# Kernel tuning notes

Measured on AMD Instinct MI355X. Metric: run time of the kernel, lower is better.

The kernel has to match this reference:

```python
import jax, jax.numpy as jnp
import numpy as np

N, D, E, TOP_K = 2048, 512, 16, 2
HID = 4 * D
EPS = 1e-10


def setup_inputs() -> dict:
    key = jax.random.key(0)
    ks = jax.random.split(key, 8)
    s = 0.02
    return {
        "x": jax.random.normal(ks[0], (N, D), dtype=jnp.float32),
        "w_norm": jnp.ones((D,), dtype=jnp.float32),
        "Wr": jax.random.normal(ks[1], (D, E), dtype=jnp.float32) * s,
        "br": jnp.zeros((E,), dtype=jnp.float32),
        "W1": jax.random.normal(ks[2], (E, D, HID), dtype=jnp.float32) * s,
        "b1": jnp.zeros((E, HID), dtype=jnp.float32),
        "W2": jax.random.normal(ks[3], (E, HID, D), dtype=jnp.float32) * s,
        "b2": jnp.zeros((E, D), dtype=jnp.float32),
    }


def reference(x, w_norm, Wr, br, W1, b1, W2, b2):
    res = x
    # RMSNorm over feature dim (dim=1 in the torch code for 2D input)
    rms = jnp.sqrt(jnp.mean(x * x, axis=1, keepdims=True) + EPS)
    xn = w_norm * (x / rms)
    # Router: top-k over expert logits, softmax over the k selected logits
    logits = xn @ Wr + br                      # [N, E]
    top_p, top_i = jax.lax.top_k(logits, TOP_K)  # [N, k]
    top_p = jax.nn.softmax(top_p, axis=-1)
    # Dense per-token expert weights [N, E] (top-k indices are distinct)
    weight = jnp.zeros((x.shape[0], E), dtype=x.dtype)
    weight = weight.at[jnp.arange(x.shape[0])[:, None], top_i].add(top_p)
    # All-expert FFN (dense reference for the routed dispatch)
    h = jnp.einsum("nd,edh->enh", xn, W1) + b1[:, None, :]   # [E, N, 4D]
    y = jnp.einsum("enh,ehd->end", jax.nn.silu(h), W2) + b2[:, None, :]  # [E, N, D]
    out = jnp.einsum("end,ne->nd", y, weight)
    return out + res
```

## Files before the change

### kernel.cpp

```cpp
#include <hip/hip_runtime.h>

#define N_TOK 2048
#define DIM   512
#define NEXP  16
#define HID   2048
#define NSLOT (N_TOK*2)

typedef __attribute__((ext_vector_type(8))) short short8;
typedef __attribute__((ext_vector_type(4))) float floatx4;

__device__ __forceinline__ ushort f2bf(float f) {
    union { float f; unsigned u; } c; c.f = f;
    unsigned u = c.u;
    unsigned r = (u + 0x7fffu + ((u >> 16) & 1u)) >> 16;
    return (ushort)r;
}
__device__ __forceinline__ float bf2f(ushort u) {
    union { unsigned u; float f; } c; c.u = ((unsigned)u) << 16;
    return c.f;
}

__device__ __forceinline__ void gl_lds16(const void* g, void* l) {
    __builtin_amdgcn_global_load_lds(
        (const __attribute__((address_space(1))) unsigned int*)g,
        (__attribute__((address_space(3))) unsigned int*)l, 16, 0, 0);
}

__global__ __launch_bounds__(256)
void transpose_convert(const float* __restrict__ src, ushort* __restrict__ dst,
                       int K, int Nn)
{
    const int NT = Nn >> 6, KT = K >> 6;
    int bx = blockIdx.x;
    const int nt = bx % NT; bx /= NT;
    const int kt = bx % KT; bx /= KT;
    const int e  = bx;

    __shared__ float Ls[64 * 65];
    const int t = threadIdx.x;

    const float* sp = src + ((size_t)e * K + kt * 64) * Nn + nt * 64;
#pragma unroll
    for (int i = 0; i < 4; i++) {
        const int k  = (t >> 4) + i * 16;
        const int c4 = (t & 15) * 4;
        const float4 v = *(const float4*)(sp + (size_t)k * Nn + c4);
        Ls[k * 65 + c4 + 0] = v.x;
        Ls[k * 65 + c4 + 1] = v.y;
        Ls[k * 65 + c4 + 2] = v.z;
        Ls[k * 65 + c4 + 3] = v.w;
    }
    __syncthreads();

    ushort* dp = dst + ((size_t)e * Nn + nt * 64) * K + kt * 64;
#pragma unroll
    for (int i = 0; i < 2; i++) {
        const int n = (t >> 3) + i * 32;
        const int c = t & 7;
        unsigned w[4];
#pragma unroll
        for (int q = 0; q < 4; q++) {
            const unsigned lo = f2bf(Ls[(c * 8 + q * 2 + 0) * 65 + n]);
            const unsigned hi = f2bf(Ls[(c * 8 + q * 2 + 1) * 65 + n]);
            w[q] = lo | (hi << 16);
        }
        uint4 o = make_uint4(w[0], w[1], w[2], w[3]);
        *(uint4*)(dp + (size_t)n * K + c * 8) = o;
    }
}

__global__ __launch_bounds__(256)
void router_fused(const float* __restrict__ x, const float* __restrict__ w_norm,
                  const float* __restrict__ Wr, const float* __restrict__ br,
                  ushort* __restrict__ xn, int2* __restrict__ rec_e,
                  float2* __restrict__ rec_w)
{
    __shared__ float xs[16][516];
    __shared__ float wrT[16][516];

    const int tid  = threadIdx.x;
    const int wave = tid >> 6, lane = tid & 63;
    const int tblk = blockIdx.x * 16;

#pragma unroll
    for (int k = 0; k < 32; k++) {
        const int idx = tid + k * 256;
        wrT[idx & 15][idx >> 4] = Wr[idx];
    }

    const float4* wnp = (const float4*)w_norm;
    const float4 wa = wnp[lane], wb = wnp[lane + 64];
#pragma unroll
    for (int i = 0; i < 4; i++) {
        const int tl = wave * 4 + i, t = tblk + tl;
        const float4* xp = (const float4*)(x + (size_t)t * DIM);
        const float4 a = xp[lane], b = xp[lane + 64];
        float ss = a.x*a.x + a.y*a.y + a.z*a.z + a.w*a.w
                 + b.x*b.x + b.y*b.y + b.z*b.z + b.w*b.w;
#pragma unroll
        for (int m = 32; m >= 1; m >>= 1) ss += __shfl_xor(ss, m, 64);
        const float rinv = 1.f / sqrtf(ss * (1.f / (float)DIM) + 1e-10f);
        float4 na, nb;
        na.x = a.x * wa.x * rinv; na.y = a.y * wa.y * rinv;
        na.z = a.z * wa.z * rinv; na.w = a.w * wa.w * rinv;
        nb.x = b.x * wb.x * rinv; nb.y = b.y * wb.y * rinv;
        nb.z = b.z * wb.z * rinv; nb.w = b.w * wb.w * rinv;
        *(float4*)&xs[tl][lane * 4]       = na;
        *(float4*)&xs[tl][256 + lane * 4] = nb;
        ushort4 ua, ub;
        ua.x = f2bf(na.x); ua.y = f2bf(na.y); ua.z = f2bf(na.z); ua.w = f2bf(na.w);
        ub.x = f2bf(nb.x); ub.y = f2bf(nb.y); ub.z = f2bf(nb.z); ub.w = f2bf(nb.w);
        ushort4* xo = (ushort4*)(xn + (size_t)t * DIM);
        xo[lane] = ua; xo[lane + 64] = ub;
    }
    __syncthreads();

    const int tl = tid >> 4, e = tid & 15;
    const int t = tblk + tl;
    float acc = 0.f;
#pragma unroll 4
    for (int d = 0; d < DIM; d += 4) {
        const float4 xv = *(const float4*)&xs[tl][d];
        const float4 wv = *(const float4*)&wrT[e][d];
        acc += xv.x * wv.x + xv.y * wv.y + xv.z * wv.z + xv.w * wv.w;
    }
    const float v = acc + br[e];

    float m0 = v; int i0 = e; float m1 = -1e30f; int i1 = 16;
#pragma unroll
    for (int msk = 1; msk < 16; msk <<= 1) {
        const float om0 = __shfl_xor(m0, msk, 64); const int oi0 = __shfl_xor(i0, msk, 64);
        const float om1 = __shfl_xor(m1, msk, 64); const int oi1 = __shfl_xor(i1, msk, 64);
        const bool bf_ = (om0 > m0) || (om0 == m0 && oi0 < i0);
        const float t0m = bf_ ? om0 : m0; const int t0i = bf_ ? oi0 : i0;
        const float l0m = bf_ ? m0 : om0; const int l0i = bf_ ? i0 : oi0;
        const bool b2_ = (om1 > m1) || (om1 == m1 && oi1 < i1);
        const float t2m = b2_ ? om1 : m1; const int t2i = b2_ ? oi1 : i1;
        const bool lw = (l0m > t2m) || (l0m == t2m && l0i < t2i);
        m0 = t0m; i0 = t0i;
        m1 = lw ? l0m : t2m; i1 = lw ? l0i : t2i;
    }
    if (e == 0) {
        const float ex = expf(m1 - m0);
        const float w0 = 1.f / (1.f + ex);
        rec_e[t] = make_int2(i0, i1);
        rec_w[t] = make_float2(w0, ex * w0);
    }
}

__global__ __launch_bounds__(1024)
void plan_kernel(const int2* __restrict__ rec_e, int* __restrict__ cnt,
                 int* __restrict__ off, int* __restrict__ tok_of_slot,
                 int* __restrict__ rec_slot)
{
    __shared__ int soff[17];
    const int e = threadIdx.x >> 6;
    const int lane = threadIdx.x & 63;

    int total = 0;
    for (int c = 0; c < N_TOK / 64; c++) {
        const int2 er = rec_e[c * 64 + lane];
        const bool hit = (er.x == e) || (er.y == e);
        total += __popcll(__ballot(hit));
    }
    if (lane == 0) soff[e + 1] = total;
    __syncthreads();
    if (threadIdx.x == 0) {
        soff[0] = 0;
        for (int q = 1; q <= 16; q++) soff[q] += soff[q - 1];
    }
    __syncthreads();
    int base = soff[e];
    if (lane == 0) { cnt[e] = soff[e + 1] - base; off[e] = base; }

    for (int c = 0; c < N_TOK / 64; c++) {
        const int t = c * 64 + lane;
        const int2 er = rec_e[t];
        const bool hit = (er.x == e) || (er.y == e);
        const unsigned long long b = __ballot(hit);
        if (hit) {
            const int slot = base + __popcll(b & ((1ull << lane) - 1ull));
            tok_of_slot[slot] = t;
            const int which = (er.y == e) ? 1 : 0;
            rec_slot[t * 2 + which] = slot;
        }
        base += __popcll(b);
    }
}

template<int MODE>
__global__ __launch_bounds__(256)
void gemm_expert(const ushort* __restrict__ A, int a_stride,
                 const ushort* __restrict__ WT, int wt_k,
                 const float* __restrict__ bias,
                 const int* __restrict__ cnt, const int* __restrict__ off,
                 const int* __restrict__ tok_of_slot,
                 ushort* __restrict__ hout, ushort* __restrict__ yout)
{
    const int flat = blockIdx.x + (blockIdx.y << 5);
    const int x = flat & 7;
    const int g = flat >> 3;
    int e, mt, nb, z;
    if (MODE == 0) {
        e  = x + ((g >> 7) << 3);
        const int r = g & 127;
        nb = r & 31; mt = r >> 5; z = 0;
    } else {
        const int G = ((g >> 5) << 3) + x;
        e = G >> 2; z = G & 3;
        const int idx = g & 31;
        mt = idx >> 3; nb = idx & 7;
    }

    const int count = cnt[e];
    if (mt * 128 >= count) return;
    const int base = off[e];
    const int rows = min(128, count - mt * 128);
    const int n0   = nb * 64;
    const int Nn   = (MODE == 0) ? HID : DIM;
    const int kbeg = (MODE == 0) ? 0 : (z * 512);
    ushort* yp = (MODE == 0) ? nullptr : (yout + (size_t)z * NSLOT * DIM);

    __shared__ __align__(16) ushort As[2][128 * 32];
    __shared__ __align__(16) ushort Bs[2][64 * 32];
    __shared__ int toks[128];

    const int tid = threadIdx.x;
    if (tid < 128) {
        const int r = tid < rows ? tid : rows - 1;
        const int slot = base + mt * 128 + r;
        toks[tid] = (MODE == 0) ? tok_of_slot[slot] : slot;
    }
    __syncthreads();

    const int lane = tid & 63;
    const int wid  = tid >> 6;
    const int wm = wid >> 1, wn = wid & 1;
    const int fr = lane & 15, fg = lane >> 4;

    const int rl  = lane >> 2;
    const int sko = ((lane & 3) ^ ((lane >> 4) & 3)) * 8;

    const ushort* aptr[2];
    const ushort* wbase = WT + (size_t)e * Nn * wt_k + (size_t)n0 * wt_k;
#pragma unroll
    for (int j = 0; j < 2; j++) {
        const int s = wid * 2 + j;
        aptr[j] = A + (size_t)toks[s * 16 + rl] * a_stride + sko;
    }
    const ushort* bptr = wbase + (size_t)(wid * 16 + rl) * wt_k + sko;

    floatx4 acc[4][2];
#pragma unroll
    for (int mi = 0; mi < 4; mi++)
#pragma unroll
        for (int ni = 0; ni < 2; ni++)
#pragma unroll
            for (int r = 0; r < 4; r++) acc[mi][ni][r] = 0.f;

#define STAGE(pb, k0)                                                        \
    do {                                                                     \
        _Pragma("unroll")                                                    \
        for (int j = 0; j < 2; j++)                                          \
            gl_lds16(aptr[j] + (k0), (void*)(&As[pb][(wid * 2 + j) * 512])); \
        gl_lds16(bptr + (k0), (void*)(&Bs[pb][wid * 512]));                  \
    } while (0)

    int cur = 0;
    STAGE(0, kbeg);

    const int cxor = (fr >> 2) & 3;
    for (int kt = 0; kt < 16; kt++) {
        if (kt < 15) {
            STAGE(cur ^ 1, kbeg + (kt + 1) * 32);
            asm volatile("s_waitcnt vmcnt(3)" ::: "memory");
        } else {
            asm volatile("s_waitcnt vmcnt(0)" ::: "memory");
        }
        __builtin_amdgcn_s_barrier();
        __builtin_amdgcn_sched_barrier(0);

        __builtin_amdgcn_s_setprio(1);
        {
            const int co = (fg ^ cxor) * 8;
            short8 af[4], bfr[2];
#pragma unroll
            for (int mi = 0; mi < 4; mi++)
                af[mi] = *(const short8*)&As[cur][(wm * 64 + mi * 16 + fr) * 32 + co];
#pragma unroll
            for (int ni = 0; ni < 2; ni++)
                bfr[ni] = *(const short8*)&Bs[cur][(wn * 32 + ni * 16 + fr) * 32 + co];
#pragma unroll
            for (int mi = 0; mi < 4; mi++)
#pragma unroll
                for (int ni = 0; ni < 2; ni++)
                    acc[mi][ni] = __builtin_amdgcn_mfma_f32_16x16x32_bf16(af[mi], bfr[ni], acc[mi][ni], 0, 0, 0);
        }
        __builtin_amdgcn_s_setprio(0);

        __builtin_amdgcn_sched_barrier(0);
        __builtin_amdgcn_s_barrier();
        cur ^= 1;
    }
#undef STAGE

#pragma unroll
    for (int ni = 0; ni < 2; ni++) {
        const int gn = n0 + wn * 32 + ni * 16 + fr;
        const float bv = (MODE == 0) ? bias[e * HID + gn] : 0.f;
#pragma unroll
        for (int mi = 0; mi < 4; mi++) {
#pragma unroll
            for (int r = 0; r < 4; r++) {
                const int lm = wm * 64 + mi * 16 + fg * 4 + r;
                if (lm < rows) {
                    const int slot = base + mt * 128 + lm;
                    float v = acc[mi][ni][r];
                    if (MODE == 0) {
                        v += bv;
                        v = v / (1.f + __expf(-v));
                        hout[(size_t)slot * HID + gn] = f2bf(v);
                    } else {
                        yp[(size_t)slot * DIM + gn] = f2bf(v);
                    }
                }
            }
        }
    }
}

__global__ __launch_bounds__(128)
void gather_kernel(const float* __restrict__ x, const ushort* __restrict__ ypart,
                   const float* __restrict__ b2,
                   const int2* __restrict__ rec_e, const float2* __restrict__ rec_w,
                   const int2* __restrict__ rec_slot, float* __restrict__ out)
{
    const int t = blockIdx.x;
    const int d4 = threadIdx.x * 4;
    const int2 ei = rec_e[t];
    const float2 w = rec_w[t];
    const int2 sl = rec_slot[t];
    const float4 xv  = *(const float4*)(x  + (size_t)t * DIM + d4);
    float4 s0 = make_float4(0.f, 0.f, 0.f, 0.f);
    float4 s1 = make_float4(0.f, 0.f, 0.f, 0.f);
#pragma unroll
    for (int kc = 0; kc < 4; kc++) {
        const ushort* yp = ypart + (size_t)kc * NSLOT * DIM;
        const ushort4 a = *(const ushort4*)(yp + (size_t)sl.x * DIM + d4);
        const ushort4 b = *(const ushort4*)(yp + (size_t)sl.y * DIM + d4);
        s0.x += bf2f(a.x); s0.y += bf2f(a.y); s0.z += bf2f(a.z); s0.w += bf2f(a.w);
        s1.x += bf2f(b.x); s1.y += bf2f(b.y); s1.z += bf2f(b.z); s1.w += bf2f(b.w);
    }
    const float4 b0  = *(const float4*)(b2 + (size_t)ei.x * DIM + d4);
    const float4 b1v = *(const float4*)(b2 + (size_t)ei.y * DIM + d4);
    float4 o;
    o.x = xv.x + w.x * (s0.x + b0.x) + w.y * (s1.x + b1v.x);
    o.y = xv.y + w.x * (s0.y + b0.y) + w.y * (s1.y + b1v.y);
    o.z = xv.z + w.x * (s0.z + b0.z) + w.y * (s1.z + b1v.z);
    o.w = xv.w + w.x * (s0.w + b0.w) + w.y * (s1.w + b1v.w);
    *(float4*)(out + (size_t)t * DIM + d4) = o;
}

extern "C" void kernel_launch(void* const* d_in, const int* in_sizes, int n_in,
                              void* d_out, int out_size, void* d_ws, size_t ws_size,
                              hipStream_t stream)
{
    const float* x  = (const float*)d_in[0];
    const float* wn = (const float*)d_in[1];
    const float* Wr = (const float*)d_in[2];
    const float* br = (const float*)d_in[3];
    const float* W1 = (const float*)d_in[4];
    const float* b1 = (const float*)d_in[5];
    const float* W2 = (const float*)d_in[6];
    const float* b2 = (const float*)d_in[7];
    float* out = (float*)d_out;

    char* ws = (char*)d_ws;
    ushort* W1T   = (ushort*)(ws);
    ushort* W2T   = (ushort*)(ws + (32u << 20));
    ushort* xn    = (ushort*)(ws + (64u << 20));
    ushort* h_buf = (ushort*)(ws + (66u << 20));
    ushort* y_par = (ushort*)(ws + (82u << 20));
    char* p = ws + (114u << 20);
    int*    cnt         = (int*)p;    p += 256;
    int*    off         = (int*)p;    p += 256;
    int2*   rec_e       = (int2*)p;   p += N_TOK * 8;
    float2* rec_w       = (float2*)p; p += N_TOK * 8;
    int2*   rec_slot    = (int2*)p;   p += N_TOK * 8;
    int*    tok_of_slot = (int*)p;    p += NSLOT * 4;

    router_fused<<<N_TOK / 16, 256, 0, stream>>>(x, wn, Wr, br, xn, rec_e, rec_w);
    plan_kernel<<<1, 1024, 0, stream>>>(rec_e, cnt, off, tok_of_slot, (int*)rec_slot);

    transpose_convert<<<NEXP * 8 * 32, 256, 0, stream>>>(W1, W1T, DIM, HID);
    gemm_expert<0><<<dim3(32, 64), 256, 0, stream>>>(
        xn, DIM, W1T, DIM, b1, cnt, off, tok_of_slot, h_buf, nullptr);

    transpose_convert<<<NEXP * 32 * 8, 256, 0, stream>>>(W2, W2T, HID, DIM);
    gemm_expert<1><<<dim3(32, 64), 256, 0, stream>>>(
        h_buf, HID, W2T, HID, nullptr, cnt, off, nullptr, nullptr, y_par);

    gather_kernel<<<N_TOK, 128, 0, stream>>>(x, y_par, b2, rec_e, rec_w, rec_slot, out);
}
```

Baseline: 117.0 us.

## Fuse weight transposes into plan and GEMM1 launches to overlap independent work

The W1 transpose-convert is merged into the single-block plan kernel as extra blocks, and the W2 transpose-convert is appended as extra blocks to the first expert GEMM launch. This cuts two kernel launches and lets the independent transpose work run alongside the serial planning block and the GEMM1 tiles. Shared memory is now a raw byte buffer shared between the two roles. The plan block now uses 256 threads handling 4 experts per wave, so it runs longer on one block, and GEMM1 blocks may compete with the transpose blocks for CUs.

```diff
diff --git a/kernel.cpp b/kernel.cpp
--- a/kernel.cpp
+++ b/kernel.cpp
@@ -26,17 +26,16 @@
         (__attribute__((address_space(3))) unsigned int*)l, 16, 0, 0);
 }
 
-__global__ __launch_bounds__(256)
-void transpose_convert(const float* __restrict__ src, ushort* __restrict__ dst,
-                       int K, int Nn)
-{
-    const int NT = Nn >> 6, KT = K >> 6;
-    int bx = blockIdx.x;
+__device__ __forceinline__ void transpose_tile(const float* __restrict__ src,
+                                               ushort* __restrict__ dst,
+                                               int K, int Nn, int bx, void* smem)
+{
+    float* Ls = (float*)smem;
+    const int NT = Nn >> 6;
+    const int KT = K >> 6;
     const int nt = bx % NT; bx /= NT;
     const int kt = bx % KT; bx /= KT;
     const int e  = bx;
-
-    __shared__ float Ls[64 * 65];
     const int t = threadIdx.x;
 
     const float* sp = src + ((size_t)e * K + kt * 64) * Nn + nt * 64;
@@ -148,56 +147,71 @@
     }
 }
 
-__global__ __launch_bounds__(1024)
-void plan_kernel(const int2* __restrict__ rec_e, int* __restrict__ cnt,
-                 int* __restrict__ off, int* __restrict__ tok_of_slot,
-                 int* __restrict__ rec_slot)
-{
-    __shared__ int soff[17];
-    const int e = threadIdx.x >> 6;
-    const int lane = threadIdx.x & 63;
-
-    int total = 0;
-    for (int c = 0; c < N_TOK / 64; c++) {
-        const int2 er = rec_e[c * 64 + lane];
-        const bool hit = (er.x == e) || (er.y == e);
-        total += __popcll(__ballot(hit));
-    }
-    if (lane == 0) soff[e + 1] = total;
+__global__ __launch_bounds__(256)
+void plan_trw1_kernel(const int2* __restrict__ rec_e, int* __restrict__ cnt,
+                      int* __restrict__ off, int* __restrict__ tok_of_slot,
+                      int* __restrict__ rec_slot,
+                      const float* __restrict__ w1src, ushort* __restrict__ w1dst)
+{
+    __shared__ __align__(16) char smem[16640];
+
+    if (blockIdx.x != 0) {
+        transpose_tile(w1src, w1dst, DIM, HID, blockIdx.x - 1, smem);
+        return;
+    }
+
+    int* soff = (int*)smem;
+    const int tid = threadIdx.x;
+    const int wv = tid >> 6, lane = tid & 63;
+
+#pragma unroll
+    for (int s = 0; s < 4; s++) {
+        const int e = wv * 4 + s;
+        int total = 0;
+        for (int c = 0; c < N_TOK / 64; c++) {
+            const int2 er = rec_e[c * 64 + lane];
+            const bool hit = (er.x == e) || (er.y == e);
+            total += __popcll(__ballot(hit));
+        }
+        if (lane == 0) soff[e + 1] = total;
+    }
     __syncthreads();
-    if (threadIdx.x == 0) {
+    if (tid == 0) {
         soff[0] = 0;
         for (int q = 1; q <= 16; q++) soff[q] += soff[q - 1];
     }
     __syncthreads();
-    int base = soff[e];
-    if (lane == 0) { cnt[e] = soff[e + 1] - base; off[e] = base; }
-
-    for (int c = 0; c < N_TOK / 64; c++) {
-        const int t = c * 64 + lane;
-        const int2 er = rec_e[t];
-        const bool hit = (er.x == e) || (er.y == e);
-        const unsigned long long b = __ballot(hit);
-        if (hit) {
-            const int slot = base + __popcll(b & ((1ull << lane) - 1ull));
-            tok_of_slot[slot] = t;
-            const int which = (er.y == e) ? 1 : 0;
-            rec_slot[t * 2 + which] = slot;
-        }
-        base += __popcll(b);
+
+#pragma unroll
+    for (int s = 0; s < 4; s++) {
+        const int e = wv * 4 + s;
+        int base = soff[e];
+        if (lane == 0) { cnt[e] = soff[e + 1] - base; off[e] = base; }
+        for (int c = 0; c < N_TOK / 64; c++) {
+            const int t = c * 64 + lane;
+            const int2 er = rec_e[t];
+            const bool hit = (er.x == e) || (er.y == e);
+            const unsigned long long b = __ballot(hit);
+            if (hit) {
+                const int slot = base + __popcll(b & ((1ull << lane) - 1ull));
+                tok_of_slot[slot] = t;
+                const int which = (er.y == e) ? 1 : 0;
+                rec_slot[t * 2 + which] = slot;
+            }
+            base += __popcll(b);
+        }
     }
 }
 
 template<int MODE>
-__global__ __launch_bounds__(256)
-void gemm_expert(const ushort* __restrict__ A, int a_stride,
+__device__ __forceinline__ void gemm_body(const ushort* __restrict__ A, int a_stride,
                  const ushort* __restrict__ WT, int wt_k,
                  const float* __restrict__ bias,
                  const int* __restrict__ cnt, const int* __restrict__ off,
                  const int* __restrict__ tok_of_slot,
-                 ushort* __restrict__ hout, ushort* __restrict__ yout)
-{
-    const int flat = blockIdx.x + (blockIdx.y << 5);
+                 ushort* __restrict__ hout, ushort* __restrict__ yout,
+                 int flat, void* smem)
+{
     const int x = flat & 7;
     const int g = flat >> 3;
     int e, mt, nb, z;
@@ -221,9 +235,9 @@
     const int kbeg = (MODE == 0) ? 0 : (z * 512);
     ushort* yp = (MODE == 0) ? nullptr : (yout + (size_t)z * NSLOT * DIM);
 
-    __shared__ __align__(16) ushort As[2][128 * 32];
-    __shared__ __align__(16) ushort Bs[2][64 * 32];
-    __shared__ int toks[128];
+    ushort* As_ = (ushort*)smem;
+    ushort* Bs_ = (ushort*)((char*)smem + 16384);
+    int*    toks = (int*)((char*)smem + 24576);
 
     const int tid = threadIdx.x;
     if (tid < 128) {
@@ -258,12 +272,12 @@
 #pragma unroll
             for (int r = 0; r < 4; r++) acc[mi][ni][r] = 0.f;
 
-#define STAGE(pb, k0)                                                        \
-    do {                                                                     \
-        _Pragma("unroll")                                                    \
-        for (int j = 0; j < 2; j++)                                          \
-            gl_lds16(aptr[j] + (k0), (void*)(&As[pb][(wid * 2 + j) * 512])); \
-        gl_lds16(bptr + (k0), (void*)(&Bs[pb][wid * 512]));                  \
+#define STAGE(pb, k0)                                                              \
+    do {                                                                           \
+        _Pragma("unroll")                                                          \
+        for (int j = 0; j < 2; j++)                                                \
+            gl_lds16(aptr[j] + (k0), (void*)(&As_[(pb) * 4096 + (wid * 2 + j) * 512])); \
+        gl_lds16(bptr + (k0), (void*)(&Bs_[(pb) * 2048 + wid * 512]));             \
     } while (0)
 
     int cur = 0;
@@ -286,10 +300,10 @@
             short8 af[4], bfr[2];
 #pragma unroll
             for (int mi = 0; mi < 4; mi++)
-                af[mi] = *(const short8*)&As[cur][(wm * 64 + mi * 16 + fr) * 32 + co];
+                af[mi] = *(const short8*)&As_[cur * 4096 + (wm * 64 + mi * 16 + fr) * 32 + co];
 #pragma unroll
             for (int ni = 0; ni < 2; ni++)
-                bfr[ni] = *(const short8*)&Bs[cur][(wn * 32 + ni * 16 + fr) * 32 + co];
+                bfr[ni] = *(const short8*)&Bs_[cur * 2048 + (wn * 32 + ni * 16 + fr) * 32 + co];
 #pragma unroll
             for (int mi = 0; mi < 4; mi++)
 #pragma unroll
@@ -329,6 +343,38 @@
     }
 }
 
+__global__ __launch_bounds__(256)
+void gemm1_trw2_kernel(const ushort* __restrict__ A,
+                       const ushort* __restrict__ W1T,
+                       const float* __restrict__ b1,
+                       const int* __restrict__ cnt, const int* __restrict__ off,
+                       const int* __restrict__ tok_of_slot,
+                       ushort* __restrict__ hout,
+                       const float* __restrict__ w2src, ushort* __restrict__ w2dst)
+{
+    __shared__ __align__(16) char smem[25088];
+    if (blockIdx.y >= 64) {
+        const int bx = (blockIdx.y - 64) * 32 + blockIdx.x;
+        transpose_tile(w2src, w2dst, HID, DIM, bx, smem);
+        return;
+    }
+    const int flat = blockIdx.x + (blockIdx.y << 5);
+    gemm_body<0>(A, DIM, W1T, DIM, b1, cnt, off, tok_of_slot, hout, nullptr,
+                 flat, smem);
+}
+
+__global__ __launch_bounds__(256)
+void gemm2_kernel(const ushort* __restrict__ A,
+                  const ushort* __restrict__ W2T,
+                  const int* __restrict__ cnt, const int* __restrict__ off,
+                  ushort* __restrict__ yout)
+{
+    __shared__ __align__(16) char smem[25088];
+    const int flat = blockIdx.x + (blockIdx.y << 5);
+    gemm_body<1>(A, HID, W2T, HID, nullptr, cnt, off, nullptr, nullptr, yout,
+                 flat, smem);
+}
+
 __global__ __launch_bounds__(128)
 void gather_kernel(const float* __restrict__ x, const ushort* __restrict__ ypart,
                    const float* __restrict__ b2,
@@ -390,15 +436,14 @@
     int*    tok_of_slot = (int*)p;    p += NSLOT * 4;
 
     router_fused<<<N_TOK / 16, 256, 0, stream>>>(x, wn, Wr, br, xn, rec_e, rec_w);
-    plan_kernel<<<1, 1024, 0, stream>>>(rec_e, cnt, off, tok_of_slot, (int*)rec_slot);
-
-    transpose_convert<<<NEXP * 8 * 32, 256, 0, stream>>>(W1, W1T, DIM, HID);
-    gemm_expert<0><<<dim3(32, 64), 256, 0, stream>>>(
-        xn, DIM, W1T, DIM, b1, cnt, off, tok_of_slot, h_buf, nullptr);
-
-    transpose_convert<<<NEXP * 32 * 8, 256, 0, stream>>>(W2, W2T, HID, DIM);
-    gemm_expert<1><<<dim3(32, 64), 256, 0, stream>>>(
-        h_buf, HID, W2T, HID, nullptr, cnt, off, nullptr, nullptr, y_par);
+
+    plan_trw1_kernel<<<1 + NEXP * 8 * 32, 256, 0, stream>>>(
+        rec_e, cnt, off, tok_of_slot, (int*)rec_slot, W1, W1T);
+
+    gemm1_trw2_kernel<<<dim3(32, 192), 256, 0, stream>>>(
+        xn, W1T, b1, cnt, off, tok_of_slot, h_buf, W2, W2T);
+
+    gemm2_kernel<<<dim3(32, 64), 256, 0, stream>>>(h_buf, W2T, cnt, off, y_par);
 
     gather_kernel<<<N_TOK, 128, 0, stream>>>(x, y_par, b2, rec_e, rec_w, rec_slot, out);
 }
```

After: 116.2 us. About the same (-0.7%).

## Fuse weight fp32-to-bf16 conversion into expert GEMMs, drop transpose kernels

Applied to the files above, without the earlier changes.

Removes the two transpose_convert passes that wrote bf16 transposed copies of W1 and W2 to workspace. The expert GEMMs now stream fp32 weights straight from the original [K,N] layout into shared memory and convert them to bf16 per element while building the MFMA B fragments. This saves a full extra read and write of both weight tensors and two launches. In exchange it doubles the bytes of weight traffic per tile and adds scalar LDS reads and conversions inside the MFMA loop.

```diff
diff --git a/kernel.cpp b/kernel.cpp
--- a/kernel.cpp
+++ b/kernel.cpp
@@ -24,49 +24,6 @@
     __builtin_amdgcn_global_load_lds(
         (const __attribute__((address_space(1))) unsigned int*)g,
         (__attribute__((address_space(3))) unsigned int*)l, 16, 0, 0);
-}
-
-__global__ __launch_bounds__(256)
-void transpose_convert(const float* __restrict__ src, ushort* __restrict__ dst,
-                       int K, int Nn)
-{
-    const int NT = Nn >> 6, KT = K >> 6;
-    int bx = blockIdx.x;
-    const int nt = bx % NT; bx /= NT;
-    const int kt = bx % KT; bx /= KT;
-    const int e  = bx;
-
-    __shared__ float Ls[64 * 65];
-    const int t = threadIdx.x;
-
-    const float* sp = src + ((size_t)e * K + kt * 64) * Nn + nt * 64;
-#pragma unroll
-    for (int i = 0; i < 4; i++) {
-        const int k  = (t >> 4) + i * 16;
-        const int c4 = (t & 15) * 4;
-        const float4 v = *(const float4*)(sp + (size_t)k * Nn + c4);
-        Ls[k * 65 + c4 + 0] = v.x;
-        Ls[k * 65 + c4 + 1] = v.y;
-        Ls[k * 65 + c4 + 2] = v.z;
-        Ls[k * 65 + c4 + 3] = v.w;
-    }
-    __syncthreads();
-
-    ushort* dp = dst + ((size_t)e * Nn + nt * 64) * K + kt * 64;
-#pragma unroll
-    for (int i = 0; i < 2; i++) {
-        const int n = (t >> 3) + i * 32;
-        const int c = t & 7;
-        unsigned w[4];
-#pragma unroll
-        for (int q = 0; q < 4; q++) {
-            const unsigned lo = f2bf(Ls[(c * 8 + q * 2 + 0) * 65 + n]);
-            const unsigned hi = f2bf(Ls[(c * 8 + q * 2 + 1) * 65 + n]);
-            w[q] = lo | (hi << 16);
-        }
-        uint4 o = make_uint4(w[0], w[1], w[2], w[3]);
-        *(uint4*)(dp + (size_t)n * K + c * 8) = o;
-    }
 }
 
 __global__ __launch_bounds__(256)
@@ -190,12 +147,12 @@
 
 template<int MODE>
 __global__ __launch_bounds__(256)
-void gemm_expert(const ushort* __restrict__ A, int a_stride,
-                 const ushort* __restrict__ WT, int wt_k,
-                 const float* __restrict__ bias,
-                 const int* __restrict__ cnt, const int* __restrict__ off,
-                 const int* __restrict__ tok_of_slot,
-                 ushort* __restrict__ hout, ushort* __restrict__ yout)
+void gemm_f32b(const ushort* __restrict__ A, int a_stride,
+               const float* __restrict__ W, int NnW, int Ktot,
+               const float* __restrict__ bias,
+               const int* __restrict__ cnt, const int* __restrict__ off,
+               const int* __restrict__ tok_of_slot,
+               ushort* __restrict__ hout, ushort* __restrict__ yout)
 {
     const int flat = blockIdx.x + (blockIdx.y << 5);
     const int x = flat & 7;
@@ -217,12 +174,11 @@
     const int base = off[e];
     const int rows = min(128, count - mt * 128);
     const int n0   = nb * 64;
-    const int Nn   = (MODE == 0) ? HID : DIM;
     const int kbeg = (MODE == 0) ? 0 : (z * 512);
     ushort* yp = (MODE == 0) ? nullptr : (yout + (size_t)z * NSLOT * DIM);
 
     __shared__ __align__(16) ushort As[2][128 * 32];
-    __shared__ __align__(16) ushort Bs[2][64 * 32];
+    __shared__ __align__(16) float  Bf[2][32 * 64];
     __shared__ int toks[128];
 
     const int tid = threadIdx.x;
@@ -242,13 +198,18 @@
     const int sko = ((lane & 3) ^ ((lane >> 4) & 3)) * 8;
 
     const ushort* aptr[2];
-    const ushort* wbase = WT + (size_t)e * Nn * wt_k + (size_t)n0 * wt_k;
 #pragma unroll
     for (int j = 0; j < 2; j++) {
         const int s = wid * 2 + j;
-        aptr[j] = A + (size_t)toks[s * 16 + rl] * a_stride + sko;
-    }
-    const ushort* bptr = wbase + (size_t)(wid * 16 + rl) * wt_k + sko;
+        aptr[j] = A + (size_t)toks[s * 16 + rl] * a_stride + kbeg + sko;
+    }
+    const float* bptr[2];
+#pragma unroll
+    for (int j = 0; j < 2; j++) {
+        const int s = wid * 2 + j;
+        bptr[j] = W + ((size_t)e * Ktot + kbeg + s * 4 + (lane >> 4)) * NnW
+                    + n0 + (lane & 15) * 4;
+    }
 
     floatx4 acc[4][2];
 #pragma unroll
@@ -258,22 +219,27 @@
 #pragma unroll
             for (int r = 0; r < 4; r++) acc[mi][ni][r] = 0.f;
 
-#define STAGE(pb, k0)                                                        \
-    do {                                                                     \
-        _Pragma("unroll")                                                    \
-        for (int j = 0; j < 2; j++)                                          \
-            gl_lds16(aptr[j] + (k0), (void*)(&As[pb][(wid * 2 + j) * 512])); \
-        gl_lds16(bptr + (k0), (void*)(&Bs[pb][wid * 512]));                  \
+#define STAGE(pb, ktn)                                                             \
+    do {                                                                           \
+        const int ka = (ktn) * 32;                                                 \
+        const size_t kb = (size_t)(ktn) * 32 * NnW;                                \
+        _Pragma("unroll")                                                          \
+        for (int j = 0; j < 2; j++)                                                \
+            gl_lds16(aptr[j] + ka, (void*)(&As[pb][(wid * 2 + j) * 512]));         \
+        _Pragma("unroll")                                                          \
+        for (int j = 0; j < 2; j++)                                                \
+            gl_lds16(bptr[j] + kb, (void*)(&Bf[pb][(wid * 2 + j) * 256]));         \
     } while (0)
 
     int cur = 0;
-    STAGE(0, kbeg);
+    STAGE(0, 0);
 
     const int cxor = (fr >> 2) & 3;
+    const int bcol = wn * 32 + fr;
     for (int kt = 0; kt < 16; kt++) {
         if (kt < 15) {
-            STAGE(cur ^ 1, kbeg + (kt + 1) * 32);
-            asm volatile("s_waitcnt vmcnt(3)" ::: "memory");
+            STAGE(cur ^ 1, kt + 1);
+            asm volatile("s_waitcnt vmcnt(4)" ::: "memory");
         } else {
             asm volatile("s_waitcnt vmcnt(0)" ::: "memory");
         }
@@ -288,8 +254,13 @@
             for (int mi = 0; mi < 4; mi++)
                 af[mi] = *(const short8*)&As[cur][(wm * 64 + mi * 16 + fr) * 32 + co];
 #pragma unroll
-            for (int ni = 0; ni < 2; ni++)
-                bfr[ni] = *(const short8*)&Bs[cur][(wn * 32 + ni * 16 + fr) * 32 + co];
+            for (int ni = 0; ni < 2; ni++) {
+#pragma unroll
+                for (int j = 0; j < 8; j++) {
+                    const float f = Bf[cur][(fg * 8 + j) * 64 + bcol + ni * 16];
+                    bfr[ni][j] = (short)f2bf(f);
+                }
+            }
 #pragma unroll
             for (int mi = 0; mi < 4; mi++)
 #pragma unroll
@@ -376,12 +347,10 @@
     float* out = (float*)d_out;
 
     char* ws = (char*)d_ws;
-    ushort* W1T   = (ushort*)(ws);
-    ushort* W2T   = (ushort*)(ws + (32u << 20));
-    ushort* xn    = (ushort*)(ws + (64u << 20));
-    ushort* h_buf = (ushort*)(ws + (66u << 20));
-    ushort* y_par = (ushort*)(ws + (82u << 20));
-    char* p = ws + (114u << 20);
+    ushort* xn    = (ushort*)(ws);
+    ushort* h_buf = (ushort*)(ws + (2u  << 20));
+    ushort* y_par = (ushort*)(ws + (18u << 20));
+    char* p = ws + (40u << 20);
     int*    cnt         = (int*)p;    p += 256;
     int*    off         = (int*)p;    p += 256;
     int2*   rec_e       = (int2*)p;   p += N_TOK * 8;
@@ -390,15 +359,14 @@
     int*    tok_of_slot = (int*)p;    p += NSLOT * 4;
 
     router_fused<<<N_TOK / 16, 256, 0, stream>>>(x, wn, Wr, br, xn, rec_e, rec_w);
+
     plan_kernel<<<1, 1024, 0, stream>>>(rec_e, cnt, off, tok_of_slot, (int*)rec_slot);
 
-    transpose_convert<<<NEXP * 8 * 32, 256, 0, stream>>>(W1, W1T, DIM, HID);
-    gemm_expert<0><<<dim3(32, 64), 256, 0, stream>>>(
-        xn, DIM, W1T, DIM, b1, cnt, off, tok_of_slot, h_buf, nullptr);
-
-    transpose_convert<<<NEXP * 32 * 8, 256, 0, stream>>>(W2, W2T, HID, DIM);
-    gemm_expert<1><<<dim3(32, 64), 256, 0, stream>>>(
-        h_buf, HID, W2T, HID, nullptr, cnt, off, nullptr, nullptr, y_par);
+    gemm_f32b<0><<<dim3(32, 64), 256, 0, stream>>>(
+        xn, DIM, W1, HID, DIM, b1, cnt, off, tok_of_slot, h_buf, nullptr);
+
+    gemm_f32b<1><<<dim3(32, 64), 256, 0, stream>>>(
+        h_buf, HID, W2, DIM, HID, nullptr, cnt, off, nullptr, nullptr, y_par);
 
     gather_kernel<<<N_TOK, 128, 0, stream>>>(x, y_par, b2, rec_e, rec_w, rec_slot, out);
 }
```

Result: faster. 107.1 us (-8.5%).

## Read fp32 W1 directly in GEMM1 and fuse W2 transpose into same launch

Applied to the files above, without the earlier changes.

Removes the separate W1 transpose/convert pass. GEMM1 now streams fp32 W1 tiles straight into LDS and converts them to bf16 per element while building MFMA fragments. The W2 transpose/convert is folded into the GEMM1 launch as extra blocks, so it can overlap with GEMM1 work and one launch is dropped. The cost is twice the LDS bytes for B, scalar LDS reads plus conversion in the inner loop, and a larger shared-memory footprint that may reduce occupancy.

```diff
diff --git a/kernel.cpp b/kernel.cpp
--- a/kernel.cpp
+++ b/kernel.cpp
@@ -26,17 +26,16 @@
         (__attribute__((address_space(3))) unsigned int*)l, 16, 0, 0);
 }
 
-__global__ __launch_bounds__(256)
-void transpose_convert(const float* __restrict__ src, ushort* __restrict__ dst,
-                       int K, int Nn)
-{
-    const int NT = Nn >> 6, KT = K >> 6;
-    int bx = blockIdx.x;
+__device__ __forceinline__ void transpose_tile(const float* __restrict__ src,
+                                               ushort* __restrict__ dst,
+                                               int K, int Nn, int bx, void* smem)
+{
+    float* Ls = (float*)smem;
+    const int NT = Nn >> 6;
+    const int KT = K >> 6;
     const int nt = bx % NT; bx /= NT;
     const int kt = bx % KT; bx /= KT;
     const int e  = bx;
-
-    __shared__ float Ls[64 * 65];
     const int t = threadIdx.x;
 
     const float* sp = src + ((size_t)e * K + kt * 64) * Nn + nt * 64;
@@ -188,48 +187,43 @@
     }
 }
 
-template<int MODE>
 __global__ __launch_bounds__(256)
-void gemm_expert(const ushort* __restrict__ A, int a_stride,
-                 const ushort* __restrict__ WT, int wt_k,
-                 const float* __restrict__ bias,
-                 const int* __restrict__ cnt, const int* __restrict__ off,
-                 const int* __restrict__ tok_of_slot,
-                 ushort* __restrict__ hout, ushort* __restrict__ yout)
-{
+void gemm1_trw2(const ushort* __restrict__ A,
+                const float* __restrict__ W1, const float* __restrict__ b1,
+                const int* __restrict__ cnt, const int* __restrict__ off,
+                const int* __restrict__ tok_of_slot,
+                ushort* __restrict__ hout,
+                const float* __restrict__ w2src, ushort* __restrict__ w2dst)
+{
+    __shared__ __align__(16) char smem[33280];
+
+    if (blockIdx.y >= 64) {
+        const int bx = (blockIdx.y - 64) * 32 + blockIdx.x;
+        transpose_tile(w2src, w2dst, HID, DIM, bx, smem);
+        return;
+    }
+
     const int flat = blockIdx.x + (blockIdx.y << 5);
     const int x = flat & 7;
     const int g = flat >> 3;
-    int e, mt, nb, z;
-    if (MODE == 0) {
-        e  = x + ((g >> 7) << 3);
-        const int r = g & 127;
-        nb = r & 31; mt = r >> 5; z = 0;
-    } else {
-        const int G = ((g >> 5) << 3) + x;
-        e = G >> 2; z = G & 3;
-        const int idx = g & 31;
-        mt = idx >> 3; nb = idx & 7;
-    }
+    const int e  = x + ((g >> 7) << 3);
+    const int r0_ = g & 127;
+    const int nb = r0_ & 31, mt = r0_ >> 5;
 
     const int count = cnt[e];
     if (mt * 128 >= count) return;
     const int base = off[e];
     const int rows = min(128, count - mt * 128);
     const int n0   = nb * 64;
-    const int Nn   = (MODE == 0) ? HID : DIM;
-    const int kbeg = (MODE == 0) ? 0 : (z * 512);
-    ushort* yp = (MODE == 0) ? nullptr : (yout + (size_t)z * NSLOT * DIM);
-
-    __shared__ __align__(16) ushort As[2][128 * 32];
-    __shared__ __align__(16) ushort Bs[2][64 * 32];
-    __shared__ int toks[128];
+
+    ushort* As_ = (ushort*)smem;
+    float*  Bf_ = (float*)(smem + 16384);
+    int*    toks = (int*)(smem + 32768);
 
     const int tid = threadIdx.x;
     if (tid < 128) {
         const int r = tid < rows ? tid : rows - 1;
-        const int slot = base + mt * 128 + r;
-        toks[tid] = (MODE == 0) ? tok_of_slot[slot] : slot;
+        toks[tid] = tok_of_slot[base + mt * 128 + r];
     }
     __syncthreads();
 
@@ -242,13 +236,18 @@
     const int sko = ((lane & 3) ^ ((lane >> 4) & 3)) * 8;
 
     const ushort* aptr[2];
-    const ushort* wbase = WT + (size_t)e * Nn * wt_k + (size_t)n0 * wt_k;
 #pragma unroll
     for (int j = 0; j < 2; j++) {
         const int s = wid * 2 + j;
-        aptr[j] = A + (size_t)toks[s * 16 + rl] * a_stride + sko;
-    }
-    const ushort* bptr = wbase + (size_t)(wid * 16 + rl) * wt_k + sko;
+        aptr[j] = A + (size_t)toks[s * 16 + rl] * DIM + sko;
+    }
+    const float* bptr[2];
+#pragma unroll
+    for (int j = 0; j < 2; j++) {
+        const int s = wid * 2 + j;
+        const int cs = ((lane & 15) * 4) ^ (((s >> 1) & 1) << 4);
+        bptr[j] = W1 + ((size_t)e * DIM + s * 4 + (lane >> 4)) * HID + n0 + cs;
+    }
 
     floatx4 acc[4][2];
 #pragma unroll
@@ -258,7 +257,142 @@
 #pragma unroll
             for (int r = 0; r < 4; r++) acc[mi][ni][r] = 0.f;
 
-#define STAGE(pb, k0)                                                        \
+#define STAGE1(pb, ktn)                                                            \
+    do {                                                                           \
+        const int ka = (ktn) * 32;                                                 \
+        const size_t kb = (size_t)(ktn) * 32 * HID;                                \
+        _Pragma("unroll")                                                          \
+        for (int j = 0; j < 2; j++)                                                \
+            gl_lds16(aptr[j] + ka, (void*)(&As_[(pb) * 4096 + (wid * 2 + j) * 512])); \
+        _Pragma("unroll")                                                          \
+        for (int j = 0; j < 2; j++)                                                \
+            gl_lds16(bptr[j] + kb, (void*)(&Bf_[(pb) * 2048 + (wid * 2 + j) * 256])); \
+    } while (0)
+
+    int cur = 0;
+    STAGE1(0, 0);
+
+    const int cxor = (fr >> 2) & 3;
+    const int bbase = wn * 32 + fr;
+    const int fgx = fg & 1;
+    for (int kt = 0; kt < 16; kt++) {
+        if (kt < 15) {
+            STAGE1(cur ^ 1, kt + 1);
+            asm volatile("s_waitcnt vmcnt(4)" ::: "memory");
+        } else {
+            asm volatile("s_waitcnt vmcnt(0)" ::: "memory");
+        }
+        __builtin_amdgcn_s_barrier();
+        __builtin_amdgcn_sched_barrier(0);
+
+        __builtin_amdgcn_s_setprio(1);
+        {
+            const int co = (fg ^ cxor) * 8;
+            short8 af[4], bfr[2];
+#pragma unroll
+            for (int mi = 0; mi < 4; mi++)
+                af[mi] = *(const short8*)&As_[cur * 4096 + (wm * 64 + mi * 16 + fr) * 32 + co];
+#pragma unroll
+            for (int ni = 0; ni < 2; ni++) {
+                const int pcol = bbase + ((ni ^ fgx) << 4);
+#pragma unroll
+                for (int j = 0; j < 8; j++) {
+                    const float f = Bf_[cur * 2048 + (fg * 8 + j) * 64 + pcol];
+                    bfr[ni][j] = (short)f2bf(f);
+                }
+            }
+#pragma unroll
+            for (int mi = 0; mi < 4; mi++)
+#pragma unroll
+                for (int ni = 0; ni < 2; ni++)
+                    acc[mi][ni] = __builtin_amdgcn_mfma_f32_16x16x32_bf16(af[mi], bfr[ni], acc[mi][ni], 0, 0, 0);
+        }
+        __builtin_amdgcn_s_setprio(0);
+
+        __builtin_amdgcn_sched_barrier(0);
+        __builtin_amdgcn_s_barrier();
+        cur ^= 1;
+    }
+#undef STAGE1
+
+#pragma unroll
+    for (int ni = 0; ni < 2; ni++) {
+        const int gn = n0 + wn * 32 + ni * 16 + fr;
+        const float bv = b1[e * HID + gn];
+#pragma unroll
+        for (int mi = 0; mi < 4; mi++) {
+#pragma unroll
+            for (int r = 0; r < 4; r++) {
+                const int lm = wm * 64 + mi * 16 + fg * 4 + r;
+                if (lm < rows) {
+                    const int slot = base + mt * 128 + lm;
+                    float v = acc[mi][ni][r] + bv;
+                    v = v / (1.f + __expf(-v));
+                    hout[(size_t)slot * HID + gn] = f2bf(v);
+                }
+            }
+        }
+    }
+}
+
+__global__ __launch_bounds__(256)
+void gemm2_kernel(const ushort* __restrict__ A,
+                  const ushort* __restrict__ WT,
+                  const int* __restrict__ cnt, const int* __restrict__ off,
+                  ushort* __restrict__ yout)
+{
+    const int flat = blockIdx.x + (blockIdx.y << 5);
+    const int x = flat & 7;
+    const int g = flat >> 3;
+    const int G = ((g >> 5) << 3) + x;
+    const int e = G >> 2, z = G & 3;
+    const int idx = g & 31;
+    const int mt = idx >> 3, nb = idx & 7;
+
+    const int count = cnt[e];
+    if (mt * 128 >= count) return;
+    const int base = off[e];
+    const int rows = min(128, count - mt * 128);
+    const int n0   = nb * 64;
+    const int kbeg = z * 512;
+    ushort* yp = yout + (size_t)z * NSLOT * DIM;
+
+    __shared__ __align__(16) ushort As[2][128 * 32];
+    __shared__ __align__(16) ushort Bs[2][64 * 32];
+    __shared__ int toks[128];
+
+    const int tid = threadIdx.x;
+    if (tid < 128) {
+        const int r = tid < rows ? tid : rows - 1;
+        toks[tid] = base + mt * 128 + r;
+    }
+    __syncthreads();
+
+    const int lane = tid & 63;
+    const int wid  = tid >> 6;
+    const int wm = wid >> 1, wn = wid & 1;
+    const int fr = lane & 15, fg = lane >> 4;
+
+    const int rl  = lane >> 2;
+    const int sko = ((lane & 3) ^ ((lane >> 4) & 3)) * 8;
+
+    const ushort* aptr[2];
+#pragma unroll
+    for (int j = 0; j < 2; j++) {
+        const int s = wid * 2 + j;
+        aptr[j] = A + (size_t)toks[s * 16 + rl] * HID + kbeg + sko;
+    }
+    const ushort* bptr = WT + ((size_t)e * DIM + n0 + wid * 16 + rl) * HID + kbeg + sko;
+
+    floatx4 acc[4][2];
+#pragma unroll
+    for (int mi = 0; mi < 4; mi++)
+#pragma unroll
+        for (int ni = 0; ni < 2; ni++)
+#pragma unroll
+            for (int r = 0; r < 4; r++) acc[mi][ni][r] = 0.f;
+
+#define STAGE2(pb, k0)                                                       \
     do {                                                                     \
         _Pragma("unroll")                                                    \
         for (int j = 0; j < 2; j++)                                          \
@@ -267,12 +401,12 @@
     } while (0)
 
     int cur = 0;
-    STAGE(0, kbeg);
+    STAGE2(0, 0);
 
     const int cxor = (fr >> 2) & 3;
     for (int kt = 0; kt < 16; kt++) {
         if (kt < 15) {
-            STAGE(cur ^ 1, kbeg + (kt + 1) * 32);
+            STAGE2(cur ^ 1, (kt + 1) * 32);
             asm volatile("s_waitcnt vmcnt(3)" ::: "memory");
         } else {
             asm volatile("s_waitcnt vmcnt(0)" ::: "memory");
@@ -302,12 +436,11 @@
         __builtin_amdgcn_s_barrier();
         cur ^= 1;
     }
-#undef STAGE
+#undef STAGE2
 
 #pragma unroll
     for (int ni = 0; ni < 2; ni++) {
         const int gn = n0 + wn * 32 + ni * 16 + fr;
-        const float bv = (MODE == 0) ? bias[e * HID + gn] : 0.f;
 #pragma unroll
         for (int mi = 0; mi < 4; mi++) {
 #pragma unroll
@@ -315,14 +448,7 @@
                 const int lm = wm * 64 + mi * 16 + fg * 4 + r;
                 if (lm < rows) {
                     const int slot = base + mt * 128 + lm;
-                    float v = acc[mi][ni][r];
-                    if (MODE == 0) {
-                        v += bv;
-                        v = v / (1.f + __expf(-v));
-                        hout[(size_t)slot * HID + gn] = f2bf(v);
-                    } else {
-                        yp[(size_t)slot * DIM + gn] = f2bf(v);
-                    }
+                    yp[(size_t)slot * DIM + gn] = f2bf(acc[mi][ni][r]);
                 }
             }
         }
@@ -376,12 +502,11 @@
     float* out = (float*)d_out;
 
     char* ws = (char*)d_ws;
-    ushort* W1T   = (ushort*)(ws);
-    ushort* W2T   = (ushort*)(ws + (32u << 20));
-    ushort* xn    = (ushort*)(ws + (64u << 20));
-    ushort* h_buf = (ushort*)(ws + (66u << 20));
-    ushort* y_par = (ushort*)(ws + (82u << 20));
-    char* p = ws + (114u << 20);
+    ushort* W2T   = (ushort*)(ws);
+    ushort* xn    = (ushort*)(ws + (32u << 20));
+    ushort* h_buf = (ushort*)(ws + (34u << 20));
+    ushort* y_par = (ushort*)(ws + (50u << 20));
+    char* p = ws + (80u << 20);
     int*    cnt         = (int*)p;    p += 256;
     int*    off         = (int*)p;    p += 256;
     int2*   rec_e       = (int2*)p;   p += N_TOK * 8;
@@ -390,15 +515,13 @@
     int*    tok_of_slot = (int*)p;    p += NSLOT * 4;
 
     router_fused<<<N_TOK / 16, 256, 0, stream>>>(x, wn, Wr, br, xn, rec_e, rec_w);
+
     plan_kernel<<<1, 1024, 0, stream>>>(rec_e, cnt, off, tok_of_slot, (int*)rec_slot);
 
-    transpose_convert<<<NEXP * 8 * 32, 256, 0, stream>>>(W1, W1T, DIM, HID);
-    gemm_expert<0><<<dim3(32, 64), 256, 0, stream>>>(
-        xn, DIM, W1T, DIM, b1, cnt, off, tok_of_slot, h_buf, nullptr);
-
-    transpose_convert<<<NEXP * 32 * 8, 256, 0, stream>>>(W2, W2T, HID, DIM);
-    gemm_expert<1><<<dim3(32, 64), 256, 0, stream>>>(
-        h_buf, HID, W2T, HID, nullptr, cnt, off, nullptr, nullptr, y_par);
+    gemm1_trw2<<<dim3(32, 192), 256, 0, stream>>>(
+        xn, W1, b1, cnt, off, tok_of_slot, h_buf, W2, W2T);
+
+    gemm2_kernel<<<dim3(32, 64), 256, 0, stream>>>(h_buf, W2T, cnt, off, y_par);
 
     gather_kernel<<<N_TOK, 128, 0, stream>>>(x, y_par, b2, rec_e, rec_w, rec_slot, out);
 }
```

New measurement: 100.7 us. 14.0% less time.
